# Performance work log

Measured on AMD Instinct MI355X. Metric: run time of the kernel, lower is better.

Reference implementation:

```python
import jax, jax.numpy as jnp
import numpy as np

B, T, D = 32, 1024, 1024
N, L = 256, 768
H = 16
TE = 2048


def layernorm(x, g, b, eps=1e-5):
    m = jnp.mean(x, axis=-1, keepdims=True)
    v = jnp.var(x, axis=-1, keepdims=True)
    return (x - m) * jax.lax.rsqrt(v + eps) * g + b


def setup_inputs() -> dict:
    key = jax.random.key(0)
    ks = jax.random.split(key, 16)
    s = 0.02
    return {
        "x": jax.random.normal(ks[0], (B, T, D), jnp.float32),
        "xf": jax.random.normal(ks[1], (B, N, L), jnp.float32),
        "emb": jax.random.normal(ks[2], (B, TE), jnp.float32),
        "src_mask": jnp.ones((B, T, 1), jnp.float32),
        "cond_type": jax.random.randint(ks[3], (B, 1, 1), 0, 100),
        # LayerNorm params
        "ln_x_g": jnp.ones((D,), jnp.float32), "ln_x_b": jnp.zeros((D,), jnp.float32),
        "ln_t_g": jnp.ones((L,), jnp.float32), "ln_t_b": jnp.zeros((L,), jnp.float32),
        # Q/K/V projections
        "Wq": jax.random.normal(ks[4], (D, D), jnp.float32) * s, "bq": jnp.zeros((D,), jnp.float32),
        "Wk": jax.random.normal(ks[5], (L, D), jnp.float32) * s, "bk": jnp.zeros((D,), jnp.float32),
        "Wv": jax.random.normal(ks[6], (L, D), jnp.float32) * s, "bv": jnp.zeros((D,), jnp.float32),
        # StylizationBlock: SiLU -> Linear(TE, 2D); LayerNorm(D); SiLU -> Linear(D, D)
        "We": jax.random.normal(ks[7], (TE, 2 * D), jnp.float32) * s, "be": jnp.zeros((2 * D,), jnp.float32),
        "ln_y_g": jnp.ones((D,), jnp.float32), "ln_y_b": jnp.zeros((D,), jnp.float32),
        "Wo": jax.random.normal(ks[8], (D, D), jnp.float32) * s, "bo": jnp.zeros((D,), jnp.float32),
    }


def reference(x, xf, emb, src_mask, cond_type,
              ln_x_g, ln_x_b, ln_t_g, ln_t_b,
              Wq, bq, Wk, bk, Wv, bv,
              We, be, ln_y_g, ln_y_b, Wo, bo):
    Bh, Th, Dh = x.shape
    Nn = xf.shape[1]
    head = Dh // H

    # text condition gate: (B,1,1), constant per batch element
    tcond = (cond_type % 10 > 0).astype(x.dtype).reshape(Bh, 1, 1)

    q = (layernorm(x, ln_x_g, ln_x_b) @ Wq + bq).reshape(Bh, Th, H, head)
    xf_n = layernorm(xf, ln_t_g, ln_t_b)
    k = (xf_n @ Wk + bk).reshape(Bh, Nn, H, head)

    # B,T,N,H scores (note: no 1/sqrt(d) scaling, as in the original)
    att = jnp.einsum('bthd,bnhd->btnh', q, k)
    att = att + (1.0 - tcond.reshape(Bh, 1, 1, 1)) * -1000000.0
    att = jax.nn.softmax(att, axis=2)

    v = ((xf_n @ Wv + bv) * tcond).reshape(Bh, Nn, H, head)
    y = jnp.einsum('btnh,bnhd->bthd', att, v).reshape(Bh, Th, Dh)

    # StylizationBlock (dropout inactive in eval)
    emb_out = jax.nn.silu(emb) @ We + be            # B, 2D
    scale, shift = jnp.split(emb_out, 2, axis=-1)   # B, D each
    h = layernorm(y, ln_y_g, ln_y_b) * (1.0 + scale[:, None, :]) + shift[:, None, :]
    h = jax.nn.silu(h) @ Wo + bo
    return x + h
```

## Files before the change

### kernel.cpp

```cpp
#include <hip/hip_runtime.h>
#include <hip/hip_bf16.h>

#define DEV __device__ __forceinline__

typedef __attribute__((ext_vector_type(8))) short bf16x8;
typedef __attribute__((ext_vector_type(4))) float f32x4;
typedef __attribute__((ext_vector_type(8))) unsigned short u16x8;

DEV unsigned short f2bf(float f){
  unsigned int b = __float_as_uint(f);
  return (unsigned short)((b + 0x7fffu + ((b >> 16) & 1u)) >> 16);
}
DEV float bf2f(unsigned short u){ return __uint_as_float(((unsigned int)u)<<16); }

DEV float silu_f(float v){ return v / (1.f + __expf(-v)); }

DEV void gl_lds16(const void* g, void* l){
  __builtin_amdgcn_global_load_lds((const __attribute__((address_space(1))) void*)g,
                                   (__attribute__((address_space(3))) void*)l, 16, 0, 0);
}

DEV void wtile(const float* W, unsigned short* Wt, int K, int N, int nt, int kt, int tid,
               float (*tile)[33])
{
  int n0 = nt<<5, k0 = kt<<5;
  int tx = tid & 31, ty = tid >> 5;
  #pragma unroll
  for (int i=0;i<4;i++)
    tile[ty + i*8][tx] = W[(size_t)(k0 + ty + i*8)*N + n0 + tx];
  __syncthreads();
  #pragma unroll
  for (int i=0;i<4;i++)
    Wt[(size_t)(n0 + ty + i*8)*K + k0 + tx] = f2bf(tile[tx][ty + i*8]);
}

__global__ __launch_bounds__(256) void prep_ln(
    const float* __restrict__ x, const float* __restrict__ xf,
    const float* __restrict__ gx, const float* __restrict__ bx_,
    const float* __restrict__ gt, const float* __restrict__ bt,
    unsigned short* __restrict__ ox, unsigned short* __restrict__ ot,
    const float* __restrict__ Wq, const float* __restrict__ Wk,
    const float* __restrict__ Wv, const float* __restrict__ Wo,
    const float* __restrict__ bk, const float* __restrict__ bv,
    unsigned short* __restrict__ wqt, unsigned short* __restrict__ wkvt,
    unsigned short* __restrict__ wot, float* __restrict__ bkv)
{
  __shared__ float shbuf[1088];
  int blk = blockIdx.x, t = threadIdx.x;
  if (blk >= 10240){
    int id = blk - 10240;
    if (id < 8){
      int i = id*256 + t;
      bkv[i] = (i < 1024) ? bk[i] : bv[i-1024];
      return;
    }
    id -= 8;
    float (*tile)[33] = (float(*)[33])shbuf;
    if (id < 1024){ wtile(Wq, wqt, 1024, 1024, id & 31, id >> 5, t, tile); return; }
    id -= 1024;
    if (id < 768){ wtile(Wk, wkvt, 768, 1024, id & 31, id >> 5, t, tile); return; }
    id -= 768;
    if (id < 768){ wtile(Wv, wkvt + (size_t)1024*768, 768, 1024, id & 31, id >> 5, t, tile); return; }
    id -= 768;
    wtile(Wo, wot, 1024, 1024, id & 31, id >> 5, t, tile);
    return;
  }
  const float* src; const float* g; const float* bb; unsigned short* out;
  int D, nvec;
  if (blk < 8192){
    int r0 = blk<<2;
    src = x + (size_t)r0*1024; g = gx; bb = bx_; out = ox + (size_t)r0*1024; D = 1024; nvec = 256;
  } else {
    int r0 = (blk-8192)<<2;
    src = xf + (size_t)r0*768; g = gt; bb = bt; out = ot + (size_t)r0*768; D = 768; nvec = 192;
  }
  float4 v[4];
  float s[4], s2[4];
  #pragma unroll
  for (int r=0;r<4;r++){
    v[r] = make_float4(0.f,0.f,0.f,0.f);
    if (t < nvec) v[r] = ((const float4*)(src + (size_t)r*D))[t];
    s[r]  = v[r].x+v[r].y+v[r].z+v[r].w;
    s2[r] = v[r].x*v[r].x+v[r].y*v[r].y+v[r].z*v[r].z+v[r].w*v[r].w;
  }
  #pragma unroll
  for (int o=32;o;o>>=1){
    #pragma unroll
    for (int r=0;r<4;r++){
      s[r]  += __shfl_down(s[r], o, 64);
      s2[r] += __shfl_down(s2[r], o, 64);
    }
  }
  int w = t>>6;
  if ((t&63)==0){
    #pragma unroll
    for (int r=0;r<4;r++){ shbuf[w*4+r] = s[r]; shbuf[16+w*4+r] = s2[r]; }
  }
  __syncthreads();
  float4 gv = make_float4(0.f,0.f,0.f,0.f), bv4 = make_float4(0.f,0.f,0.f,0.f);
  if (t < nvec){ gv = ((const float4*)g)[t]; bv4 = ((const float4*)bb)[t]; }
  float invD = 1.f/(float)D;
  #pragma unroll
  for (int r=0;r<4;r++){
    float fs  = shbuf[r] + shbuf[4+r] + shbuf[8+r] + shbuf[12+r];
    float fs2 = shbuf[16+r] + shbuf[20+r] + shbuf[24+r] + shbuf[28+r];
    float mean = fs*invD;
    float var  = fmaxf(fs2*invD - mean*mean, 0.f);
    float rstd = rsqrtf(var + 1e-5f);
    if (t < nvec){
      ushort4 o4;
      o4.x = f2bf((v[r].x-mean)*rstd*gv.x + bv4.x);
      o4.y = f2bf((v[r].y-mean)*rstd*gv.y + bv4.y);
      o4.z = f2bf((v[r].z-mean)*rstd*gv.z + bv4.z);
      o4.w = f2bf((v[r].w-mean)*rstd*gv.w + bv4.w);
      *(ushort4*)(out + (size_t)r*D + t*4) = o4;
    }
  }
}

__global__ __launch_bounds__(256) void embgemm(const float* __restrict__ emb,
    const float* __restrict__ We, float* __restrict__ epart)
{
  __shared__ float a[32][128];
  int cb = blockIdx.x, ks = blockIdx.y, tid = threadIdx.x;
  int k0 = ks<<7;
  #pragma unroll
  for (int it=0; it<4; ++it){
    int fi = it*256 + tid;
    int r = fi>>5, c4 = (fi&31)<<2;
    float4 vv = *(const float4*)(emb + (size_t)r*2048 + k0 + c4);
    vv.x = silu_f(vv.x); vv.y = silu_f(vv.y); vv.z = silu_f(vv.z); vv.w = silu_f(vv.w);
    *(float4*)&a[r][c4] = vv;
  }
  __syncthreads();
  int c0 = (cb<<8) + tid;
  float acc[32];
  #pragma unroll
  for (int r=0;r<32;r++) acc[r]=0.f;
  #pragma unroll 4
  for (int kk=0;kk<128;kk++){
    float wv = We[(size_t)(k0+kk)*2048 + c0];
    #pragma unroll
    for (int r=0;r<32;r++) acc[r] += a[r][kk]*wv;
  }
  #pragma unroll
  for (int r=0;r<32;r++) epart[(size_t)(ks*32 + r)*2048 + c0] = acc[r];
}

template<int EPI>
DEV void gemm_body(
  const unsigned char* __restrict__ A, const unsigned char* __restrict__ Wt,
  const float* __restrict__ bias, void* __restrict__ Cout,
  const float* __restrict__ Xadd, unsigned char* __restrict__ vt,
  int M, int N, int K, int bx, int by, unsigned char* lds)
{
  const int tid = threadIdx.x, w = tid>>6, lane = tid&63;
  const int l15 = lane&15, lq = lane>>4;
  const int m0 = by<<7, n0 = bx<<7;
  const size_t K2 = (size_t)K<<1;
  const int KT = K>>6;
  const int wr = (w>>1)&1, wc = w&1;
  const int srow = lane>>3;
  const int scb  = (lane&7)<<4;

  f32x4 acc[4][4];
  f32x4 zero = {0.f,0.f,0.f,0.f};
  #pragma unroll
  for (int i=0;i<4;i++)
    #pragma unroll
    for (int j=0;j<4;j++) acc[i][j] = zero;

  auto stage = [&](int buf, int kt){
    unsigned char* ldsA = lds + buf*32768;
    const size_t kb = (size_t)kt<<7;
    #pragma unroll
    for (int inst=0; inst<4; ++inst){
      int base = w*1024 + inst*4096;
      int row  = (base>>7) + srow;
      int cs   = scb ^ ((row&7)<<4);
      gl_lds16(A  + (size_t)(m0+row)*K2 + kb + cs, ldsA + base);
      gl_lds16(Wt + (size_t)(n0+row)*K2 + kb + cs, ldsA + 16384 + base);
    }
  };

  stage(0, 0);
  __syncthreads();
  for (int kt=0; kt<KT; ++kt){
    if (kt+1 < KT) stage((kt+1)&1, kt+1);
    const unsigned char* ldsA = lds + (kt&1)*32768;
    const unsigned char* ldsB = ldsA + 16384;
    bf16x8 af[2][4], bfr[2][4];
    #pragma unroll
    for (int i=0;i<4;i++){
      int r = wr*64 + i*16 + l15;
      int rb = r<<7, sw = (r&7)<<4;
      af[0][i] = *(const bf16x8*)(ldsA + rb + ((lq*16) ^ sw));
      af[1][i] = *(const bf16x8*)(ldsA + rb + ((64 + lq*16) ^ sw));
    }
    #pragma unroll
    for (int j=0;j<4;j++){
      int r = wc*64 + j*16 + l15;
      int rb = r<<7, sw = (r&7)<<4;
      bfr[0][j] = *(const bf16x8*)(ldsB + rb + ((lq*16) ^ sw));
      bfr[1][j] = *(const bf16x8*)(ldsB + rb + ((64 + lq*16) ^ sw));
    }
    #pragma unroll
    for (int kc=0;kc<2;kc++)
      #pragma unroll
      for (int i=0;i<4;i++)
        #pragma unroll
        for (int j=0;j<4;j++)
          acc[i][j] = __builtin_amdgcn_mfma_f32_16x16x32_bf16(af[kc][i], bfr[kc][j], acc[i][j], 0,0,0);
    __syncthreads();
  }
  #pragma unroll
  for (int j=0;j<4;j++){
    int n = n0 + wc*64 + j*16 + l15;
    float bvs = bias[n];
    #pragma unroll
    for (int i=0;i<4;i++){
      int mb = m0 + wr*64 + i*16 + lq*4;
      #pragma unroll
      for (int r=0;r<4;r++){
        int m = mb + r;
        float val = acc[i][j][r] + bvs;
        if (EPI==0){
          ((unsigned short*)Cout)[(size_t)m*N + n] = f2bf(val);
        } else if (EPI==1){
          size_t idx = (size_t)m*N + n;
          ((float*)Cout)[idx] = Xadd[idx] + val;
        } else {
          if (n0 < 1024){
            ((unsigned short*)Cout)[(size_t)m*1024 + n] = f2bf(val);
          } else {
            int d  = (n-1024)&63;
            int hh = (n-1024)>>6;
            int bb_ = m>>8, nk = m&255;
            *(unsigned short*)(vt + ((size_t)(bb_*16+hh)<<15) + d*512
                + (((nk>>3)<<4) ^ ((d&7)<<4)) + ((nk&7)<<1)) = f2bf(val);
          }
        }
      }
    }
  }
}

__global__ __launch_bounds__(256,2) void qkv(
  const unsigned char* __restrict__ xln, const unsigned char* __restrict__ wqt,
  const float* __restrict__ bq, unsigned char* __restrict__ qb,
  const unsigned char* __restrict__ xfn, const unsigned char* __restrict__ wkvt,
  const float* __restrict__ bkv, unsigned char* __restrict__ kb,
  unsigned char* __restrict__ vtb,
  const float* __restrict__ epart, const float* __restrict__ be,
  float* __restrict__ eo)
{
  __shared__ __align__(16) unsigned char lds[65536];
  int wg = blockIdx.x;
  if (wg < 2048){
    int lg = (wg & 7) * 256 + (wg >> 3);
    gemm_body<0>(xln, wqt, bq, qb, nullptr, nullptr, 32768, 1024, 1024, lg & 7, lg >> 3, lds);
  } else if (wg < 3072){
    int w2 = wg - 2048;
    int lg = (w2 & 7) * 128 + (w2 >> 3);
    gemm_body<2>(xfn, wkvt, bkv, kb, nullptr, vtb, 8192, 2048, 768, lg & 15, lg >> 4, lds);
  } else {
    int idx0 = (wg - 3072) * 2048 + threadIdx.x;
    #pragma unroll
    for (int e=0;e<8;e++){
      int idx = idx0 + e*256;
      float s = be[idx & 2047];
      #pragma unroll
      for (int ks=0;ks<16;ks++) s += epart[(size_t)ks*65536 + idx];
      eo[idx] = s;
    }
  }
}

__global__ __launch_bounds__(256,2) void attn64(
  const unsigned char* __restrict__ qg, const unsigned char* __restrict__ kg,
  int kstride, const unsigned char* __restrict__ vtg, const int* __restrict__ cond,
  unsigned short* __restrict__ yout)
{
  __shared__ __align__(16) unsigned char lds[73728];
  const int wg = blockIdx.x;
  const int lg = (wg & 7) * 1024 + (wg >> 3);
  const int t0 = (lg & 15) * 64;
  const int h  = (lg >> 4) & 15;
  const int b  = lg >> 8;
  const int tid = threadIdx.x, w = tid>>6, lane = tid&63;
  const int l15 = lane&15, lq = lane>>4;

  if (cond[b] % 10 == 0){
    int row = t0 + (tid>>2);
    unsigned short* dst = yout + (size_t)(b*1024 + row)*1024 + h*64 + (tid&3)*16;
    u16x8 z = {0,0,0,0,0,0,0,0};
    *(u16x8*)dst = z;
    *(u16x8*)(dst + 8) = z;
    return;
  }

  const unsigned char* kbase = kg + (size_t)b*256*kstride + (size_t)h*128;
  const unsigned char* vtb   = vtg + (size_t)(b*16+h)*32768;
  #pragma unroll
  for (int i=0;i<8;i++){
    int base = (w*8+i)*1024;
    int n  = (base>>7) + (lane>>3);
    int cb = (lane&7)<<4;
    gl_lds16(kbase + (size_t)n*kstride + (cb ^ ((n&7)<<4)), lds + base);
    gl_lds16(vtb + base + lane*16, lds + 32768 + base);
  }
  const unsigned char* qbase = qg + (size_t)(b*1024 + t0)*2048 + h*128;
  #pragma unroll
  for (int i=0;i<2;i++){
    int row = i*32 + (tid>>3);
    int cs  = ((tid&7)<<4) ^ ((row&7)<<4);
    gl_lds16(qbase + (size_t)row*2048 + cs, lds + 65536 + i*4096 + w*1024);
  }
  __syncthreads();

  const int qr = w*16 + l15;
  const int qsw = (qr&7)<<4;
  bf16x8 aq0 = *(const bf16x8*)(lds + 65536 + qr*128 + ((lq*16) ^ qsw));
  bf16x8 aq1 = *(const bf16x8*)(lds + 65536 + qr*128 + ((64 + lq*16) ^ qsw));

  f32x4 zero = {0.f,0.f,0.f,0.f};
  f32x4 s[16];
  #pragma unroll
  for (int nt=0;nt<16;nt++) s[nt] = zero;
  #pragma unroll
  for (int nt=0;nt<16;nt++){
    int n = nt*16 + l15;
    int rb = n<<7, sw = (n&7)<<4;
    bf16x8 kb0 = *(const bf16x8*)(lds + rb + ((lq*16) ^ sw));
    bf16x8 kb1 = *(const bf16x8*)(lds + rb + ((64 + lq*16) ^ sw));
    s[nt] = __builtin_amdgcn_mfma_f32_16x16x32_bf16(aq0, kb0, s[nt], 0,0,0);
    s[nt] = __builtin_amdgcn_mfma_f32_16x16x32_bf16(aq1, kb1, s[nt], 0,0,0);
  }
  #pragma unroll
  for (int r=0;r<4;r++){
    float m = s[0][r];
    #pragma unroll
    for (int nt=1;nt<16;nt++) m = fmaxf(m, s[nt][r]);
    m = fmaxf(m, __shfl_xor(m,1,64));
    m = fmaxf(m, __shfl_xor(m,2,64));
    m = fmaxf(m, __shfl_xor(m,4,64));
    m = fmaxf(m, __shfl_xor(m,8,64));
    float sum = 0.f;
    #pragma unroll
    for (int nt=0;nt<16;nt++){ float p = __expf(s[nt][r]-m); s[nt][r]=p; sum+=p; }
    sum += __shfl_xor(sum,1,64);
    sum += __shfl_xor(sum,2,64);
    sum += __shfl_xor(sum,4,64);
    sum += __shfl_xor(sum,8,64);
    float inv = 1.f/sum;
    #pragma unroll
    for (int nt=0;nt<16;nt++) s[nt][r] *= inv;
  }
  __syncthreads();
  #pragma unroll
  for (int nt=0;nt<16;nt++){
    int n = nt*16 + l15;
    int nb = (n>>3)<<4, nr = (n&7)<<1;
    #pragma unroll
    for (int r=0;r<4;r++){
      int tl = w*16 + lq*4 + r;
      *(unsigned short*)(lds + tl*512 + ((nb ^ ((tl&7)<<4)) | nr)) = f2bf(s[nt][r]);
    }
  }
  __syncthreads();
  f32x4 yv[4];
  #pragma unroll
  for (int dt=0;dt<4;dt++) yv[dt] = zero;
  const int tl = w*16 + l15;
  const int swp = (tl&7)<<4;
  #pragma unroll
  for (int kc=0;kc<8;kc++){
    bf16x8 pa = *(const bf16x8*)(lds + tl*512 + ((kc*64 + lq*16) ^ swp));
    #pragma unroll
    for (int dt=0;dt<4;dt++){
      int d = dt*16 + l15;
      bf16x8 vbv = *(const bf16x8*)(lds + 32768 + d*512 + ((kc*64 + lq*16) ^ ((d&7)<<4)));
      yv[dt] = __builtin_amdgcn_mfma_f32_16x16x32_bf16(pa, vbv, yv[dt], 0,0,0);
    }
  }
  #pragma unroll
  for (int dt=0;dt<4;dt++){
    #pragma unroll
    for (int r=0;r<4;r++){
      int tt = t0 + w*16 + lq*4 + r;
      yout[(size_t)(b*1024 + tt)*1024 + h*64 + dt*16 + l15] = f2bf(yv[dt][r]);
    }
  }
}

__global__ __launch_bounds__(256) void styl(const unsigned short* __restrict__ y,
    const float* __restrict__ g, const float* __restrict__ bt,
    const float* __restrict__ eo, unsigned short* __restrict__ hout)
{
  int row = blockIdx.x, t = threadIdx.x, b = row>>10;
  ushort4 yv4 = ((const ushort4*)(y + (size_t)row*1024))[t];
  float in[4] = {bf2f(yv4.x), bf2f(yv4.y), bf2f(yv4.z), bf2f(yv4.w)};
  float s  = in[0]+in[1]+in[2]+in[3];
  float s2 = in[0]*in[0]+in[1]*in[1]+in[2]*in[2]+in[3]*in[3];
  #pragma unroll
  for (int o=32;o;o>>=1){ s += __shfl_down(s,o,64); s2 += __shfl_down(s2,o,64); }
  __shared__ float red[8];
  if ((t&63)==0){ red[t>>6]=s; red[4+(t>>6)]=s2; }
  __syncthreads();
  float fs  = red[0]+red[1]+red[2]+red[3];
  float fs2 = red[4]+red[5]+red[6]+red[7];
  float mean = fs*(1.f/1024.f);
  float var  = fmaxf(fs2*(1.f/1024.f) - mean*mean, 0.f);
  float rstd = rsqrtf(var + 1e-5f);
  float4 gv = ((const float4*)g)[t];
  float4 bv = ((const float4*)bt)[t];
  float4 sc = ((const float4*)(eo + (size_t)b*2048))[t];
  float4 sh = ((const float4*)(eo + (size_t)b*2048 + 1024))[t];
  float gg[4]  = {gv.x,gv.y,gv.z,gv.w};
  float bb[4]  = {bv.x,bv.y,bv.z,bv.w};
  float scs[4] = {sc.x,sc.y,sc.z,sc.w};
  float shs[4] = {sh.x,sh.y,sh.z,sh.w};
  unsigned short oo[4];
  #pragma unroll
  for (int c=0;c<4;c++){
    float hv = (in[c]-mean)*rstd*gg[c] + bb[c];
    hv = hv*(1.f+scs[c]) + shs[c];
    oo[c] = f2bf(silu_f(hv));
  }
  ushort4 o4; o4.x=oo[0]; o4.y=oo[1]; o4.z=oo[2]; o4.w=oo[3];
  *(ushort4*)(hout + (size_t)row*1024 + t*4) = o4;
}

__global__ __launch_bounds__(256,2) void gemmO(
  const unsigned char* __restrict__ A, const unsigned char* __restrict__ Wt,
  const float* __restrict__ bias, float* __restrict__ Cout,
  const float* __restrict__ Xadd)
{
  __shared__ __align__(16) unsigned char lds[65536];
  int wg = blockIdx.x;
  int lg = (wg & 7) * 256 + (wg >> 3);
  gemm_body<1>(A, Wt, bias, Cout, Xadd, nullptr, 32768, 1024, 1024, lg & 7, lg >> 3, lds);
}

extern "C" void kernel_launch(void* const* d_in, const int* in_sizes, int n_in,
                              void* d_out, int out_size, void* d_ws, size_t ws_size,
                              hipStream_t stream) {
  const float* x      = (const float*)d_in[0];
  const float* xf     = (const float*)d_in[1];
  const float* emb    = (const float*)d_in[2];
  const int*   cond   = (const int*)d_in[4];
  const float* ln_x_g = (const float*)d_in[5];
  const float* ln_x_b = (const float*)d_in[6];
  const float* ln_t_g = (const float*)d_in[7];
  const float* ln_t_b = (const float*)d_in[8];
  const float* Wq     = (const float*)d_in[9];
  const float* bq     = (const float*)d_in[10];
  const float* Wk     = (const float*)d_in[11];
  const float* bk     = (const float*)d_in[12];
  const float* Wv     = (const float*)d_in[13];
  const float* bv     = (const float*)d_in[14];
  const float* We     = (const float*)d_in[15];
  const float* be     = (const float*)d_in[16];
  const float* ln_y_g = (const float*)d_in[17];
  const float* ln_y_b = (const float*)d_in[18];
  const float* Wo     = (const float*)d_in[19];
  const float* bo     = (const float*)d_in[20];
  float* out = (float*)d_out;

  unsigned char* ws = (unsigned char*)d_ws;
  size_t off = 0;
  auto take = [&](size_t n){ unsigned char* p = ws + off; off += (n + 255) & ~(size_t)255; return p; };
  unsigned char* r1    = take(67108864);
  unsigned char* qb    = take(67108864);
  unsigned char* xfn   = take(12582912);
  unsigned char* kb    = take(16777216);
  unsigned char* vtb   = take(16777216);
  unsigned char* wqt   = take(2097152);
  unsigned char* wkvt  = take(3145728);
  unsigned char* wot   = take(2097152);
  unsigned char* eo    = take(262144);
  unsigned char* bkv   = take(8192);
  unsigned char* epart = take(4194304);

  dim3 blk(256);
  prep_ln<<<13832, blk, 0, stream>>>(x, xf, ln_x_g, ln_x_b, ln_t_g, ln_t_b,
      (unsigned short*)r1, (unsigned short*)xfn,
      Wq, Wk, Wv, Wo, bk, bv,
      (unsigned short*)wqt, (unsigned short*)wkvt, (unsigned short*)wot, (float*)bkv);
  embgemm<<<dim3(8,16), blk, 0, stream>>>(emb, We, (float*)epart);
  qkv<<<3104, blk, 0, stream>>>(r1, wqt, bq, qb,
      xfn, wkvt, (const float*)bkv, kb, vtb,
      (const float*)epart, be, (float*)eo);
  attn64<<<8192, blk, 0, stream>>>(qb, kb, 2048, vtb, cond, (unsigned short*)qb);
  styl<<<32768, blk, 0, stream>>>((const unsigned short*)qb, ln_y_g, ln_y_b, (const float*)eo, (unsigned short*)r1);
  gemmO<<<2048, blk, 0, stream>>>(r1, wot, bo, out, x);
}
```

Baseline: 430.2 us.

## Skip QKV GEMM tiles for gated-off batches and merge emb kernels

```diff
diff --git a/kernel.cpp b/kernel.cpp
--- a/kernel.cpp
+++ b/kernel.cpp
@@ -43,9 +43,11 @@
     const float* __restrict__ Wv, const float* __restrict__ Wo,
     const float* __restrict__ bk, const float* __restrict__ bv,
     unsigned short* __restrict__ wqt, unsigned short* __restrict__ wkvt,
-    unsigned short* __restrict__ wot, float* __restrict__ bkv)
-{
-  __shared__ float shbuf[1088];
+    unsigned short* __restrict__ wot, float* __restrict__ bkv,
+    const float* __restrict__ emb, const float* __restrict__ We,
+    float* __restrict__ epart)
+{
+  __shared__ float shbuf[4096];
   int blk = blockIdx.x, t = threadIdx.x;
   if (blk >= 10240){
     int id = blk - 10240;
@@ -55,14 +57,42 @@
       return;
     }
     id -= 8;
-    float (*tile)[33] = (float(*)[33])shbuf;
-    if (id < 1024){ wtile(Wq, wqt, 1024, 1024, id & 31, id >> 5, t, tile); return; }
-    id -= 1024;
-    if (id < 768){ wtile(Wk, wkvt, 768, 1024, id & 31, id >> 5, t, tile); return; }
-    id -= 768;
-    if (id < 768){ wtile(Wv, wkvt + (size_t)1024*768, 768, 1024, id & 31, id >> 5, t, tile); return; }
-    id -= 768;
-    wtile(Wo, wot, 1024, 1024, id & 31, id >> 5, t, tile);
+    if (id < 3584){
+      float (*tile)[33] = (float(*)[33])shbuf;
+      if (id < 1024){ wtile(Wq, wqt, 1024, 1024, id & 31, id >> 5, t, tile); return; }
+      id -= 1024;
+      if (id < 768){ wtile(Wk, wkvt, 768, 1024, id & 31, id >> 5, t, tile); return; }
+      id -= 768;
+      if (id < 768){ wtile(Wv, wkvt + (size_t)1024*768, 768, 1024, id & 31, id >> 5, t, tile); return; }
+      id -= 768;
+      wtile(Wo, wot, 1024, 1024, id & 31, id >> 5, t, tile);
+      return;
+    }
+    id -= 3584;
+    float (*a)[128] = (float(*)[128])shbuf;
+    int cb = id & 7, ks = id >> 3;
+    int k0 = ks << 7;
+    #pragma unroll
+    for (int it=0; it<4; ++it){
+      int fi = it*256 + t;
+      int r = fi>>5, c4 = (fi&31)<<2;
+      float4 vv = *(const float4*)(emb + (size_t)r*2048 + k0 + c4);
+      vv.x = silu_f(vv.x); vv.y = silu_f(vv.y); vv.z = silu_f(vv.z); vv.w = silu_f(vv.w);
+      *(float4*)&a[r][c4] = vv;
+    }
+    __syncthreads();
+    int c0 = (cb<<8) + t;
+    float accv[32];
+    #pragma unroll
+    for (int r=0;r<32;r++) accv[r]=0.f;
+    #pragma unroll 4
+    for (int kk=0;kk<128;kk++){
+      float wv = We[(size_t)(k0+kk)*2048 + c0];
+      #pragma unroll
+      for (int r=0;r<32;r++) accv[r] += a[r][kk]*wv;
+    }
+    #pragma unroll
+    for (int r=0;r<32;r++) epart[(size_t)(ks*32 + r)*2048 + c0] = accv[r];
     return;
   }
   const float* src; const float* g; const float* bb; unsigned short* out;
@@ -116,35 +146,6 @@
       *(ushort4*)(out + (size_t)r*D + t*4) = o4;
     }
   }
-}
-
-__global__ __launch_bounds__(256) void embgemm(const float* __restrict__ emb,
-    const float* __restrict__ We, float* __restrict__ epart)
-{
-  __shared__ float a[32][128];
-  int cb = blockIdx.x, ks = blockIdx.y, tid = threadIdx.x;
-  int k0 = ks<<7;
-  #pragma unroll
-  for (int it=0; it<4; ++it){
-    int fi = it*256 + tid;
-    int r = fi>>5, c4 = (fi&31)<<2;
-    float4 vv = *(const float4*)(emb + (size_t)r*2048 + k0 + c4);
-    vv.x = silu_f(vv.x); vv.y = silu_f(vv.y); vv.z = silu_f(vv.z); vv.w = silu_f(vv.w);
-    *(float4*)&a[r][c4] = vv;
-  }
-  __syncthreads();
-  int c0 = (cb<<8) + tid;
-  float acc[32];
-  #pragma unroll
-  for (int r=0;r<32;r++) acc[r]=0.f;
-  #pragma unroll 4
-  for (int kk=0;kk<128;kk++){
-    float wv = We[(size_t)(k0+kk)*2048 + c0];
-    #pragma unroll
-    for (int r=0;r<32;r++) acc[r] += a[r][kk]*wv;
-  }
-  #pragma unroll
-  for (int r=0;r<32;r++) epart[(size_t)(ks*32 + r)*2048 + c0] = acc[r];
 }
 
 template<int EPI>
@@ -250,21 +251,36 @@
   const float* __restrict__ bq, unsigned char* __restrict__ qb,
   const unsigned char* __restrict__ xfn, const unsigned char* __restrict__ wkvt,
   const float* __restrict__ bkv, unsigned char* __restrict__ kb,
-  unsigned char* __restrict__ vtb,
-  const float* __restrict__ epart, const float* __restrict__ be,
-  float* __restrict__ eo)
+  unsigned char* __restrict__ vtb, const int* __restrict__ cond)
 {
   __shared__ __align__(16) unsigned char lds[65536];
   int wg = blockIdx.x;
   if (wg < 2048){
     int lg = (wg & 7) * 256 + (wg >> 3);
-    gemm_body<0>(xln, wqt, bq, qb, nullptr, nullptr, 32768, 1024, 1024, lg & 7, lg >> 3, lds);
-  } else if (wg < 3072){
+    int by = lg >> 3;
+    if (cond[by >> 3] % 10 == 0) return;
+    gemm_body<0>(xln, wqt, bq, qb, nullptr, nullptr, 32768, 1024, 1024, lg & 7, by, lds);
+  } else {
     int w2 = wg - 2048;
     int lg = (w2 & 7) * 128 + (w2 >> 3);
-    gemm_body<2>(xfn, wkvt, bkv, kb, nullptr, vtb, 8192, 2048, 768, lg & 15, lg >> 4, lds);
-  } else {
-    int idx0 = (wg - 3072) * 2048 + threadIdx.x;
+    int by = lg >> 4;
+    if (cond[by >> 1] % 10 == 0) return;
+    gemm_body<2>(xfn, wkvt, bkv, kb, nullptr, vtb, 8192, 2048, 768, lg & 15, by, lds);
+  }
+}
+
+__global__ __launch_bounds__(256,2) void attn64(
+  const unsigned char* __restrict__ qg, const unsigned char* __restrict__ kg,
+  int kstride, const unsigned char* __restrict__ vtg, const int* __restrict__ cond,
+  unsigned short* __restrict__ yout,
+  const float* __restrict__ epart, const float* __restrict__ be,
+  float* __restrict__ eo)
+{
+  __shared__ __align__(16) unsigned char lds[73728];
+  const int wg = blockIdx.x;
+  const int tid = threadIdx.x;
+  if (wg >= 8192){
+    int idx0 = (wg - 8192) * 2048 + tid;
     #pragma unroll
     for (int e=0;e<8;e++){
       int idx = idx0 + e*256;
@@ -273,21 +289,13 @@
       for (int ks=0;ks<16;ks++) s += epart[(size_t)ks*65536 + idx];
       eo[idx] = s;
     }
-  }
-}
-
-__global__ __launch_bounds__(256,2) void attn64(
-  const unsigned char* __restrict__ qg, const unsigned char* __restrict__ kg,
-  int kstride, const unsigned char* __restrict__ vtg, const int* __restrict__ cond,
-  unsigned short* __restrict__ yout)
-{
-  __shared__ __align__(16) unsigned char lds[73728];
-  const int wg = blockIdx.x;
+    return;
+  }
   const int lg = (wg & 7) * 1024 + (wg >> 3);
   const int t0 = (lg & 15) * 64;
   const int h  = (lg >> 4) & 15;
   const int b  = lg >> 8;
-  const int tid = threadIdx.x, w = tid>>6, lane = tid&63;
+  const int w = tid>>6, lane = tid&63;
   const int l15 = lane&15, lq = lane>>4;
 
   if (cond[b] % 10 == 0){
@@ -483,15 +491,15 @@
   unsigned char* epart = take(4194304);
 
   dim3 blk(256);
-  prep_ln<<<13832, blk, 0, stream>>>(x, xf, ln_x_g, ln_x_b, ln_t_g, ln_t_b,
+  prep_ln<<<13960, blk, 0, stream>>>(x, xf, ln_x_g, ln_x_b, ln_t_g, ln_t_b,
       (unsigned short*)r1, (unsigned short*)xfn,
       Wq, Wk, Wv, Wo, bk, bv,
-      (unsigned short*)wqt, (unsigned short*)wkvt, (unsigned short*)wot, (float*)bkv);
-  embgemm<<<dim3(8,16), blk, 0, stream>>>(emb, We, (float*)epart);
-  qkv<<<3104, blk, 0, stream>>>(r1, wqt, bq, qb,
-      xfn, wkvt, (const float*)bkv, kb, vtb,
+      (unsigned short*)wqt, (unsigned short*)wkvt, (unsigned short*)wot, (float*)bkv,
+      emb, We, (float*)epart);
+  qkv<<<3072, blk, 0, stream>>>(r1, wqt, bq, qb,
+      xfn, wkvt, (const float*)bkv, kb, vtb, cond);
+  attn64<<<8224, blk, 0, stream>>>(qb, kb, 2048, vtb, cond, (unsigned short*)qb,
       (const float*)epart, be, (float*)eo);
-  attn64<<<8192, blk, 0, stream>>>(qb, kb, 2048, vtb, cond, (unsigned short*)qb);
   styl<<<32768, blk, 0, stream>>>((const unsigned short*)qb, ln_y_g, ln_y_b, (const float*)eo, (unsigned short*)r1);
   gemmO<<<2048, blk, 0, stream>>>(r1, wot, bo, out, x);
 }
```

Measured after the change: 467.2 us. 1.09x slower.
